# Kernel tuning notes

Measured on AMD Instinct MI355X. Metric: run time of the kernel, lower is better.

## Reference

```python
import jax, jax.numpy as jnp
import numpy as np

B, T, TREF, NBINS, H = 4096, 8192, 8192, 50, 32  # np.linspace(lo,hi,50) -> 49 bins
EPS = 1e-10


def setup_inputs() -> dict:
    key = jax.random.key(0)
    k0, k1, k2, k3, k4, k5 = jax.random.split(key, 6)
    return {
        "current_returns": jax.random.normal(k0, (B, T), jnp.float32) * 0.02,
        "reference_returns": jax.random.normal(k1, (TREF,), jnp.float32) * 0.02,
        "w1": jax.random.normal(k2, (H, 1), jnp.float32) * 0.5,   # Linear(1, H).weight
        "b1": jax.random.normal(k3, (H,), jnp.float32) * 0.1,
        "w2": jax.random.normal(k4, (H, H), jnp.float32) * 0.1,   # Linear(H, H).weight
        "b2": jax.random.normal(k5, (H,), jnp.float32) * 0.1,
    }


def _kl_from_hists(ref, curr, ref_min, ref_max):
    # Faithful to InformationTheory.kl_divergence with n_bins=50 (49 equal-width bins).
    nb = NBINS - 1
    lo = jnp.minimum(ref_min, curr.min())
    hi = jnp.maximum(ref_max, curr.max())
    width = (hi - lo) / nb

    def hist_density(x):
        # np.histogram(x, bins=linspace(lo,hi,50), density=True); all x in [lo,hi],
        # right edge goes to last bin (handled by clip).
        idx = jnp.clip(jnp.floor((x - lo) / width).astype(jnp.int32), 0, nb - 1)
        counts = jnp.zeros(nb, jnp.float32).at[idx].add(1.0)
        return counts / (x.shape[0] * width)

    p = hist_density(ref) + EPS
    q = hist_density(curr) + EPS
    p = p / p.sum()
    q = q / q.sum()
    return jnp.sum(p * jnp.log(p / q))


def reference(current_returns, reference_returns, w1, b1, w2, b2):
    ref = reference_returns
    ref_min, ref_max = ref.min(), ref.max()
    kl = jax.vmap(lambda c: _kl_from_hists(ref, c, ref_min, ref_max))(current_returns)  # [B]
    kl = jax.lax.stop_gradient(kl)  # original detaches before building kl_tensor
    x = kl[:, None]                                  # [B, 1]
    h = jax.nn.relu(x @ w1.T + b1)                   # [B, H]
    encoded = h @ w2.T + b2                          # [B, H]
    return kl, encoded
```

## Files before the change

kernel.cpp:

```cpp
#include <hip/hip_runtime.h>
#include <math.h>

constexpr int T_LEN  = 8192;
constexpr int B_ROWS = 4096;
constexpr int NB     = 49;
constexpr int NC     = 32;
constexpr int HDIM   = 32;
constexpr float EPSF = 1e-10f;

__global__ __launch_bounds__(256)
void ref_minmax_kernel(const float* __restrict__ ref, float* __restrict__ ws) {
    __shared__ float smn[256], smx[256];
    int tid = threadIdx.x;
    float mn = 3.0e38f, mx = -3.0e38f;
    const float4* r4 = (const float4*)ref;
    for (int i = tid; i < T_LEN / 4; i += 256) {
        float4 v = r4[i];
        mn = fminf(mn, fminf(fminf(v.x, v.y), fminf(v.z, v.w)));
        mx = fmaxf(mx, fmaxf(fmaxf(v.x, v.y), fmaxf(v.z, v.w)));
    }
    smn[tid] = mn; smx[tid] = mx;
    __syncthreads();
    for (int s = 128; s > 0; s >>= 1) {
        if (tid < s) {
            smn[tid] = fminf(smn[tid], smn[tid + s]);
            smx[tid] = fmaxf(smx[tid], smx[tid + s]);
        }
        __syncthreads();
    }
    if (tid == 0) { ws[0] = smn[0]; ws[1] = smx[0]; }
}

__global__ __launch_bounds__(256)
void kl_fused_kernel(const float* __restrict__ cur,
                     const float* __restrict__ ref,
                     const float* __restrict__ ws,
                     const float* __restrict__ w1,
                     const float* __restrict__ b1,
                     const float* __restrict__ w2,
                     const float* __restrict__ b2,
                     float* __restrict__ kl_out,
                     float* __restrict__ enc_out) {
    __shared__ unsigned hp[NC * NB], hq[NC * NB];
    __shared__ float rmn[4], rmx[4];

    const int b    = blockIdx.x;
    const int tid  = threadIdx.x;
    const int lane = tid & 63;
    const int wave = tid >> 6;

    for (int i = tid; i < NC * NB; i += 256) { hp[i] = 0u; hq[i] = 0u; }

    const float4* src = (const float4*)(cur + (size_t)b * T_LEN);
    float4 v[8];
    float mn = 3.0e38f, mx = -3.0e38f;
    #pragma unroll
    for (int i = 0; i < 8; ++i) {
        v[i] = src[tid + i * 256];
        mn = fminf(mn, fminf(fminf(v[i].x, v[i].y), fminf(v[i].z, v[i].w)));
        mx = fmaxf(mx, fmaxf(fmaxf(v[i].x, v[i].y), fmaxf(v[i].z, v[i].w)));
    }
    #pragma unroll
    for (int off = 32; off > 0; off >>= 1) {
        mn = fminf(mn, __shfl_xor(mn, off));
        mx = fmaxf(mx, __shfl_xor(mx, off));
    }
    if (lane == 0) { rmn[wave] = mn; rmx[wave] = mx; }
    __syncthreads();

    const float cmin = fminf(fminf(rmn[0], rmn[1]), fminf(rmn[2], rmn[3]));
    const float cmax = fmaxf(fmaxf(rmx[0], rmx[1]), fmaxf(rmx[2], rmx[3]));
    const float lo = fminf(ws[0], cmin);
    const float hi = fmaxf(ws[1], cmax);
    const float width = (hi - lo) / (float)NB;

    unsigned* myq = hq + (tid & (NC - 1)) * NB;
    #pragma unroll
    for (int i = 0; i < 8; ++i) {
        int i0 = min(max((int)floorf((v[i].x - lo) / width), 0), NB - 1);
        int i1 = min(max((int)floorf((v[i].y - lo) / width), 0), NB - 1);
        int i2 = min(max((int)floorf((v[i].z - lo) / width), 0), NB - 1);
        int i3 = min(max((int)floorf((v[i].w - lo) / width), 0), NB - 1);
        atomicAdd(&myq[i0], 1u);
        atomicAdd(&myq[i1], 1u);
        atomicAdd(&myq[i2], 1u);
        atomicAdd(&myq[i3], 1u);
    }
    unsigned* myp = hp + (tid & (NC - 1)) * NB;
    const float4* r4 = (const float4*)ref;
    #pragma unroll
    for (int i = 0; i < 8; ++i) {
        float4 rv = r4[tid + i * 256];
        int i0 = min(max((int)floorf((rv.x - lo) / width), 0), NB - 1);
        int i1 = min(max((int)floorf((rv.y - lo) / width), 0), NB - 1);
        int i2 = min(max((int)floorf((rv.z - lo) / width), 0), NB - 1);
        int i3 = min(max((int)floorf((rv.w - lo) / width), 0), NB - 1);
        atomicAdd(&myp[i0], 1u);
        atomicAdd(&myp[i1], 1u);
        atomicAdd(&myp[i2], 1u);
        atomicAdd(&myp[i3], 1u);
    }
    __syncthreads();

    if (tid < 64) {
        const bool act = tid < NB;
        float p = 0.0f, q = 0.0f;
        if (act) {
            unsigned sp = 0u, sq = 0u;
            #pragma unroll
            for (int c = 0; c < NC; ++c) { sp += hp[c * NB + tid]; sq += hq[c * NB + tid]; }
            const float inv = 1.0f / ((float)T_LEN * width);
            p = (float)sp * inv + EPSF;
            q = (float)sq * inv + EPSF;
        }
        float P = p, Q = q;
        #pragma unroll
        for (int off = 32; off > 0; off >>= 1) {
            P += __shfl_xor(P, off);
            Q += __shfl_xor(Q, off);
        }
        float term = 0.0f;
        if (act) {
            const float pn = p / P;
            const float qn = q / Q;
            term = pn * logf(pn / qn);
        }
        #pragma unroll
        for (int off = 32; off > 0; off >>= 1) term += __shfl_xor(term, off);
        if (tid == 0) kl_out[b] = term;

        if (tid < HDIM) {
            const float k = term;
            float acc = b2[tid];
            #pragma unroll
            for (int t = 0; t < HDIM; ++t) {
                float h = fmaxf(fmaf(k, w1[t], b1[t]), 0.0f);
                acc = fmaf(h, w2[tid * HDIM + t], acc);
            }
            enc_out[(size_t)b * HDIM + tid] = acc;
        }
    }
}

extern "C" void kernel_launch(void* const* d_in, const int* in_sizes, int n_in,
                              void* d_out, int out_size, void* d_ws, size_t ws_size,
                              hipStream_t stream) {
    const float* cur = (const float*)d_in[0];
    const float* ref = (const float*)d_in[1];
    const float* w1  = (const float*)d_in[2];
    const float* b1  = (const float*)d_in[3];
    const float* w2  = (const float*)d_in[4];
    const float* b2  = (const float*)d_in[5];
    float* out = (float*)d_out;
    float* ws  = (float*)d_ws;

    ref_minmax_kernel<<<1, 256, 0, stream>>>(ref, ws);
    kl_fused_kernel<<<B_ROWS, 256, 0, stream>>>(
        cur, ref, ws, w1, b1, w2, b2, out, out + B_ROWS);
}
```

Measured before the change: 46.33 us.

## Sort reference once and derive its histogram by binary search per row

Replaces the reference min/max kernel with a rank-based sort kernel that writes a sorted copy of the reference series to the workspace. Each row block then reads min and max from the ends of the sorted array and obtains the reference bin counts by binary-searching the bin edges, instead of re-binning all 8192 reference values with shared atomics for every row. It also swaps the per-element division for a multiply-add with a precomputed reciprocal. The trade-off is an O(T^2) sort pre-pass, plus a possible boundary mismatch between the binary-search edge test and the FMA-based binning.

```diff
diff --git a/kernel.cpp b/kernel.cpp
--- a/kernel.cpp
+++ b/kernel.cpp
@@ -9,39 +9,51 @@
 constexpr float EPSF = 1e-10f;
 
 __global__ __launch_bounds__(256)
-void ref_minmax_kernel(const float* __restrict__ ref, float* __restrict__ ws) {
-    __shared__ float smn[256], smx[256];
-    int tid = threadIdx.x;
-    float mn = 3.0e38f, mx = -3.0e38f;
+void rank_sort_kernel(const float* __restrict__ ref, float* __restrict__ sorted_out) {
+    __shared__ float vals[T_LEN];
+    __shared__ int   partial[256];
+    const int tid = threadIdx.x;
     const float4* r4 = (const float4*)ref;
-    for (int i = tid; i < T_LEN / 4; i += 256) {
-        float4 v = r4[i];
-        mn = fminf(mn, fminf(fminf(v.x, v.y), fminf(v.z, v.w)));
-        mx = fmaxf(mx, fmaxf(fmaxf(v.x, v.y), fmaxf(v.z, v.w)));
+    float4* v4 = (float4*)vals;
+    for (int i = tid; i < T_LEN / 4; i += 256) v4[i] = r4[i];
+    __syncthreads();
+
+    const int jpart = tid >> 4;
+    const int iloc  = tid & 15;
+    const int i     = blockIdx.x * 16 + iloc;
+    const float x   = vals[i];
+    int rank = 0;
+    const int fbase = jpart * 128;
+    const int rot   = jpart * 34;
+    for (int t = 0; t < 128; ++t) {
+        const int f = fbase + ((t + rot) & 127);
+        const float4 y = v4[f];
+        const int j = f * 4;
+        rank += (y.x < x || (y.x == x && (j + 0) < i)) ? 1 : 0;
+        rank += (y.y < x || (y.y == x && (j + 1) < i)) ? 1 : 0;
+        rank += (y.z < x || (y.z == x && (j + 2) < i)) ? 1 : 0;
+        rank += (y.w < x || (y.w == x && (j + 3) < i)) ? 1 : 0;
     }
-    smn[tid] = mn; smx[tid] = mx;
+    partial[tid] = rank;
     __syncthreads();
-    for (int s = 128; s > 0; s >>= 1) {
-        if (tid < s) {
-            smn[tid] = fminf(smn[tid], smn[tid + s]);
-            smx[tid] = fmaxf(smx[tid], smx[tid + s]);
-        }
-        __syncthreads();
+    if (tid < 16) {
+        int r = 0;
+        #pragma unroll
+        for (int jp = 0; jp < 16; ++jp) r += partial[jp * 16 + tid];
+        sorted_out[r] = vals[blockIdx.x * 16 + tid];
     }
-    if (tid == 0) { ws[0] = smn[0]; ws[1] = smx[0]; }
 }
 
 __global__ __launch_bounds__(256)
 void kl_fused_kernel(const float* __restrict__ cur,
-                     const float* __restrict__ ref,
-                     const float* __restrict__ ws,
+                     const float* __restrict__ sref,
                      const float* __restrict__ w1,
                      const float* __restrict__ b1,
                      const float* __restrict__ w2,
                      const float* __restrict__ b2,
                      float* __restrict__ kl_out,
                      float* __restrict__ enc_out) {
-    __shared__ unsigned hp[NC * NB], hq[NC * NB];
+    __shared__ unsigned hq[NC * NB];
     __shared__ float rmn[4], rmx[4];
 
     const int b    = blockIdx.x;
@@ -49,7 +61,7 @@
     const int lane = tid & 63;
     const int wave = tid >> 6;
 
-    for (int i = tid; i < NC * NB; i += 256) { hp[i] = 0u; hq[i] = 0u; }
+    for (int i = tid; i < NC * NB; i += 256) hq[i] = 0u;
 
     const float4* src = (const float4*)(cur + (size_t)b * T_LEN);
     float4 v[8];
@@ -70,47 +82,49 @@
 
     const float cmin = fminf(fminf(rmn[0], rmn[1]), fminf(rmn[2], rmn[3]));
     const float cmax = fmaxf(fmaxf(rmx[0], rmx[1]), fmaxf(rmx[2], rmx[3]));
-    const float lo = fminf(ws[0], cmin);
-    const float hi = fmaxf(ws[1], cmax);
+    const float lo = fminf(sref[0], cmin);
+    const float hi = fmaxf(sref[T_LEN - 1], cmax);
     const float width = (hi - lo) / (float)NB;
 
+    const float winv = 1.0f / width;
+    const float nlw  = -lo * winv;
     unsigned* myq = hq + (tid & (NC - 1)) * NB;
     #pragma unroll
     for (int i = 0; i < 8; ++i) {
-        int i0 = min(max((int)floorf((v[i].x - lo) / width), 0), NB - 1);
-        int i1 = min(max((int)floorf((v[i].y - lo) / width), 0), NB - 1);
-        int i2 = min(max((int)floorf((v[i].z - lo) / width), 0), NB - 1);
-        int i3 = min(max((int)floorf((v[i].w - lo) / width), 0), NB - 1);
+        int i0 = min(max((int)floorf(fmaf(v[i].x, winv, nlw)), 0), NB - 1);
+        int i1 = min(max((int)floorf(fmaf(v[i].y, winv, nlw)), 0), NB - 1);
+        int i2 = min(max((int)floorf(fmaf(v[i].z, winv, nlw)), 0), NB - 1);
+        int i3 = min(max((int)floorf(fmaf(v[i].w, winv, nlw)), 0), NB - 1);
         atomicAdd(&myq[i0], 1u);
         atomicAdd(&myq[i1], 1u);
         atomicAdd(&myq[i2], 1u);
         atomicAdd(&myq[i3], 1u);
     }
-    unsigned* myp = hp + (tid & (NC - 1)) * NB;
-    const float4* r4 = (const float4*)ref;
-    #pragma unroll
-    for (int i = 0; i < 8; ++i) {
-        float4 rv = r4[tid + i * 256];
-        int i0 = min(max((int)floorf((rv.x - lo) / width), 0), NB - 1);
-        int i1 = min(max((int)floorf((rv.y - lo) / width), 0), NB - 1);
-        int i2 = min(max((int)floorf((rv.z - lo) / width), 0), NB - 1);
-        int i3 = min(max((int)floorf((rv.w - lo) / width), 0), NB - 1);
-        atomicAdd(&myp[i0], 1u);
-        atomicAdd(&myp[i1], 1u);
-        atomicAdd(&myp[i2], 1u);
-        atomicAdd(&myp[i3], 1u);
-    }
     __syncthreads();
 
     if (tid < 64) {
         const bool act = tid < NB;
+        int C = T_LEN;
+        if (tid < NB - 1) {
+            const float kp1 = (float)(tid + 1);
+            int l = 0, r = T_LEN;
+            while (l < r) {
+                const int m = (l + r) >> 1;
+                const float xv = sref[m];
+                if ((xv - lo) / width < kp1) l = m + 1; else r = m;
+            }
+            C = l;
+        }
+        int Cprev = __shfl_up(C, 1);
+        if (tid == 0) Cprev = 0;
+
         float p = 0.0f, q = 0.0f;
         if (act) {
-            unsigned sp = 0u, sq = 0u;
+            unsigned sq = 0u;
             #pragma unroll
-            for (int c = 0; c < NC; ++c) { sp += hp[c * NB + tid]; sq += hq[c * NB + tid]; }
+            for (int c = 0; c < NC; ++c) sq += hq[c * NB + tid];
             const float inv = 1.0f / ((float)T_LEN * width);
-            p = (float)sp * inv + EPSF;
+            p = (float)(C - Cprev) * inv + EPSF;
             q = (float)sq * inv + EPSF;
         }
         float P = p, Q = q;
@@ -151,10 +165,10 @@
     const float* b1  = (const float*)d_in[3];
     const float* w2  = (const float*)d_in[4];
     const float* b2  = (const float*)d_in[5];
-    float* out = (float*)d_out;
-    float* ws  = (float*)d_ws;
+    float* out  = (float*)d_out;
+    float* sref = (float*)d_ws;
 
-    ref_minmax_kernel<<<1, 256, 0, stream>>>(ref, ws);
+    rank_sort_kernel<<<T_LEN / 16, 256, 0, stream>>>(ref, sref);
     kl_fused_kernel<<<B_ROWS, 256, 0, stream>>>(
-        cur, ref, ws, w1, b1, w2, b2, out, out + B_ROWS);
+        cur, sref, w1, b1, w2, b2, out, out + B_ROWS);
 }
```

New measurement: 67.51 us. 1.46x slower.
